# Kernel tuning notes

Measured on AMD Instinct MI355X. Metric: run time of the kernel, lower is better.

## Reference

```python
import jax, jax.numpy as jnp
import numpy as np
from jax import lax

WINDOW = 9
PAD = WINDOW // 2
LAMBDA_REG = 1.0
DN = lax.conv_dimension_numbers((1, 1, 1, 1, 1), (1, 1, 1, 1, 1), ('NCDHW', 'OIDHW', 'NCDHW'))


def _box_sum(x):
    """Sum over a 9x9x9 window with SAME padding, via separable 1D box filters.
    Mathematically identical to conv3d with an all-ones 9^3 kernel."""
    dtype = x.dtype
    for axis in range(3):  # D, H, W spatial axes
        kshape = [1, 1, 1, 1, 1]
        kshape[2 + axis] = WINDOW
        kernel = jnp.ones(kshape, dtype=dtype)
        padding = [(0, 0)] * 3
        padding[axis] = (PAD, PAD)
        x = lax.conv_general_dilated(x, kernel, window_strides=(1, 1, 1),
                                     padding=padding, dimension_numbers=DN)
    return x


def _lncc(I_fixed, I_moved):
    n = WINDOW ** 3
    fixed_sum = _box_sum(I_fixed)
    moved_sum = _box_sum(I_moved)
    fixed_mean = fixed_sum / n
    moved_mean = moved_sum / n
    fixed_sq = _box_sum(I_fixed * I_fixed)   # note: window SUM of squares (as in original)
    moved_sq = _box_sum(I_moved * I_moved)
    fixed_moved = _box_sum(I_fixed * I_moved)
    var_fixed = fixed_sq - fixed_mean ** 2
    var_moved = moved_sq - moved_mean ** 2
    cov = fixed_moved - fixed_mean * moved_mean
    cc = cov ** 2 / (var_fixed * var_moved + 1e-8)
    return -jnp.mean(cc)


def _gradient_loss(flow):
    dy = jnp.abs(flow[:, :, 1:, :, :] - flow[:, :, :-1, :, :])
    dx = jnp.abs(flow[:, :, :, 1:, :] - flow[:, :, :, :-1, :])
    dz = jnp.abs(flow[:, :, :, :, 1:] - flow[:, :, :, :, :-1])
    return jnp.mean(dx) + jnp.mean(dy) + jnp.mean(dz)


def setup_inputs() -> dict:
    key = jax.random.key(0)
    k1, k2, k3 = jax.random.split(key, 3)
    B, D, H, W = 2, 160, 192, 160
    I_fixed = jax.random.uniform(k1, (B, 1, D, H, W), dtype=jnp.float32)
    I_moved = jax.random.uniform(k2, (B, 1, D, H, W), dtype=jnp.float32)
    flow = jax.random.normal(k3, (B, 3, D, H, W), dtype=jnp.float32)
    return {"I_fixed": I_fixed, "I_moved": I_moved, "flow": flow}


def reference(I_fixed, I_moved, flow):
    L_sim = _lncc(I_fixed, I_moved)
    L_reg = _gradient_loss(flow)
    L_total = L_sim + LAMBDA_REG * L_reg
    return (L_total, L_sim, L_reg)
```

## Files before the change

kernel.cpp:

```cpp
#include <hip/hip_runtime.h>

#define Bz 2
#define Dz 160
#define Hz 192
#define Wz 160
#define HWl (Hz*Wz)
#define DHWl (Dz*Hz*Wz)

#define TH 16
#define TW 32
#define DT 32
#define RAWH (TH+8)
#define RAWW (TW+8)
#define NB_H (Hz/TH)
#define NB_W (Wz/TW)
#define NB_D (Dz/DT)
#define LNCC_BLOCKS (Bz*NB_H*NB_W*NB_D)
#define LNCC_THREADS 512
#define NSLICE (DT+8)

#define FLOW_BLOCKS 2048
#define FLOW_THREADS 256
#define FLOW_N4 ((Bz*3*DHWl)/4)

#define FPO LNCC_BLOCKS
#define WS_DOUBLES (FPO + 3*FLOW_BLOCKS)

__global__ __launch_bounds__(LNCC_THREADS, 2)
void lncc_kernel(const float* __restrict__ F, const float* __restrict__ M,
                 double* __restrict__ ws, int mode) {
    __shared__ float2 raw[RAWH][RAWW];
    __shared__ float4 wbv[RAWH][TW];
    __shared__ float  wbs[RAWH][TW];
    __shared__ double wred[LNCC_THREADS/64];

    const int bid = blockIdx.x;
    const int dc = bid % NB_D;
    const int wc = (bid / NB_D) % NB_W;
    const int hc = (bid / (NB_D * NB_W)) % NB_H;
    const int b  = bid / (NB_D * NB_W * NB_H);

    const int tid = threadIdx.x;
    const int th = tid >> 5;
    const int tw = tid & 31;

    const int h0 = hc * TH;
    const int w0 = wc * TW;
    const int d0 = dc * DT;
    const size_t bbase = (size_t)b * DHWl;

    float circ[9][5];
#pragma unroll
    for (int i = 0; i < 9; ++i)
#pragma unroll
        for (int j = 0; j < 5; ++j) circ[i][j] = 0.f;
    float rs0 = 0.f, rs1 = 0.f, rs2 = 0.f, rs3 = 0.f, rs4 = 0.f;
    float cc_acc = 0.f;

    for (int i0 = 0; i0 < NSLICE; i0 += 9) {
#pragma unroll
        for (int q = 0; q < 9; ++q) {
            const int i = i0 + q;
            if (i < NSLICE) {
                const int s = d0 - 4 + i;
                float nv0 = 0.f, nv1 = 0.f, nv2 = 0.f, nv3 = 0.f, nv4 = 0.f;
                if (s >= 0 && s < Dz) {
                    __syncthreads();
                    const size_t sbase = bbase + (size_t)s * HWl;
                    for (int k = tid; k < RAWH * RAWW; k += LNCC_THREADS) {
                        const int r = k / RAWW;
                        const int c = k - r * RAWW;
                        const int gh = h0 - 4 + r;
                        const int gw = w0 - 4 + c;
                        float fv = 0.f, mv = 0.f;
                        if (gh >= 0 && gh < Hz && gw >= 0 && gw < Wz) {
                            const size_t gi = sbase + (size_t)gh * Wz + gw;
                            fv = F[gi];
                            mv = M[gi];
                        }
                        raw[r][c] = make_float2(fv, mv);
                    }
                    __syncthreads();
                    for (int k = tid; k < RAWH * TW; k += LNCC_THREADS) {
                        const int r = k >> 5;
                        const int j = k & 31;
                        float sf = 0.f, sm = 0.f, sff = 0.f, smm = 0.f, sfm = 0.f;
#pragma unroll
                        for (int t = 0; t < 9; ++t) {
                            const float2 fm = raw[r][j + t];
                            sf  += fm.x;
                            sm  += fm.y;
                            sff += fm.x * fm.x;
                            smm += fm.y * fm.y;
                            sfm += fm.x * fm.y;
                        }
                        wbv[r][j] = make_float4(sf, sm, sff, smm);
                        wbs[r][j] = sfm;
                    }
                    __syncthreads();
#pragma unroll
                    for (int t = 0; t < 9; ++t) {
                        const float4 v = wbv[th + t][tw];
                        nv0 += v.x; nv1 += v.y; nv2 += v.z; nv3 += v.w;
                        nv4 += wbs[th + t][tw];
                    }
                }
                rs0 += nv0 - circ[q][0]; circ[q][0] = nv0;
                rs1 += nv1 - circ[q][1]; circ[q][1] = nv1;
                rs2 += nv2 - circ[q][2]; circ[q][2] = nv2;
                rs3 += nv3 - circ[q][3]; circ[q][3] = nv3;
                rs4 += nv4 - circ[q][4]; circ[q][4] = nv4;
                if (i >= 8) {
                    const float inv_n = 1.0f / 729.0f;
                    const float mf   = rs0 * inv_n;
                    const float mm   = rs1 * inv_n;
                    const float varf = rs2 - mf * mf;
                    const float varm = rs3 - mm * mm;
                    const float cov  = rs4 - mf * mm;
                    const float cc = cov * cov / (varf * varm + 1e-8f);
                    cc_acc += cc;
                }
            }
        }
    }

    double v = (double)cc_acc;
#pragma unroll
    for (int off = 32; off > 0; off >>= 1) v += __shfl_down(v, off);
    const int wave = tid >> 6, lane = tid & 63;
    if (lane == 0) wred[wave] = v;
    __syncthreads();
    if (tid == 0) {
        double t = 0.0;
        for (int k = 0; k < LNCC_THREADS / 64; ++k) t += wred[k];
        if (mode) ws[bid] = t;
        else      atomicAdd(&ws[0], t);
    }
}

__global__ __launch_bounds__(FLOW_THREADS)
void flow_grad_kernel(const float* __restrict__ X, double* __restrict__ ws, int mode) {
    __shared__ double wr0[4], wr1[4], wr2[4];
    float sd = 0.f, sh = 0.f, sw = 0.f;
    const int stride = gridDim.x * blockDim.x;
    for (int i4 = blockIdx.x * blockDim.x + threadIdx.x; i4 < FLOW_N4; i4 += stride) {
        const int base = i4 * 4;
        const float4 v = *(const float4*)(X + base);
        const int pos  = base % DHWl;
        const int w    = pos % Wz;
        const int rest = pos / Wz;
        const int h    = rest % Hz;
        const int d    = rest / Hz;
        float s = fabsf(v.y - v.x) + fabsf(v.z - v.y) + fabsf(v.w - v.z);
        if (w > 0) s += fabsf(v.x - X[base - 1]);
        sw += s;
        if (h > 0) {
            const float4 u = *(const float4*)(X + base - Wz);
            sh += fabsf(v.x - u.x) + fabsf(v.y - u.y) + fabsf(v.z - u.z) + fabsf(v.w - u.w);
        }
        if (d > 0) {
            const float4 u = *(const float4*)(X + base - HWl);
            sd += fabsf(v.x - u.x) + fabsf(v.y - u.y) + fabsf(v.z - u.z) + fabsf(v.w - u.w);
        }
    }
    double a = (double)sd, b = (double)sh, c = (double)sw;
#pragma unroll
    for (int off = 32; off > 0; off >>= 1) {
        a += __shfl_down(a, off);
        b += __shfl_down(b, off);
        c += __shfl_down(c, off);
    }
    const int wave = threadIdx.x >> 6, lane = threadIdx.x & 63;
    if (lane == 0) { wr0[wave] = a; wr1[wave] = b; wr2[wave] = c; }
    __syncthreads();
    if (threadIdx.x == 0) {
        double ta = 0.0, tb = 0.0, tc = 0.0;
        for (int k = 0; k < 4; ++k) { ta += wr0[k]; tb += wr1[k]; tc += wr2[k]; }
        if (mode) {
            double* p = ws + FPO + 3 * (size_t)blockIdx.x;
            p[0] = ta; p[1] = tb; p[2] = tc;
        } else {
            atomicAdd(&ws[1], ta);
            atomicAdd(&ws[2], tb);
            atomicAdd(&ws[3], tc);
        }
    }
}

__global__ __launch_bounds__(512)
void finalize_kernel(const double* __restrict__ ws, float* __restrict__ out, int mode) {
    __shared__ double red[4][8];
    double cc = 0.0, sd = 0.0, sh = 0.0, sw = 0.0;
    const int tid = threadIdx.x;
    if (mode) {
        for (int i = tid; i < LNCC_BLOCKS; i += 512) cc += ws[i];
        for (int i = tid; i < FLOW_BLOCKS; i += 512) {
            const double* p = ws + FPO + 3 * (size_t)i;
            sd += p[0]; sh += p[1]; sw += p[2];
        }
    } else if (tid == 0) {
        cc = ws[0]; sd = ws[1]; sh = ws[2]; sw = ws[3];
    }
#pragma unroll
    for (int off = 32; off > 0; off >>= 1) {
        cc += __shfl_down(cc, off);
        sd += __shfl_down(sd, off);
        sh += __shfl_down(sh, off);
        sw += __shfl_down(sw, off);
    }
    const int wave = tid >> 6, lane = tid & 63;
    if (lane == 0) { red[0][wave] = cc; red[1][wave] = sd; red[2][wave] = sh; red[3][wave] = sw; }
    __syncthreads();
    if (tid == 0) {
        double tcc = 0.0, tsd = 0.0, tsh = 0.0, tsw = 0.0;
        for (int k = 0; k < 8; ++k) {
            tcc += red[0][k]; tsd += red[1][k]; tsh += red[2][k]; tsw += red[3][k];
        }
        const double n_cc = 9830400.0;
        const double n_dx = 29337600.0;
        const double n_dy = 29306880.0;
        const double n_dz = 29306880.0;
        const double L_sim = -tcc / n_cc;
        const double L_reg = tsh / n_dx + tsd / n_dy + tsw / n_dz;
        out[0] = (float)(L_sim + L_reg);
        out[1] = (float)L_sim;
        out[2] = (float)L_reg;
    }
}

extern "C" void kernel_launch(void* const* d_in, const int* in_sizes, int n_in,
                              void* d_out, int out_size, void* d_ws, size_t ws_size,
                              hipStream_t stream) {
    (void)in_sizes; (void)n_in; (void)out_size;
    const float* F = (const float*)d_in[0];
    const float* M = (const float*)d_in[1];
    const float* X = (const float*)d_in[2];
    double* ws = (double*)d_ws;
    float* out = (float*)d_out;

    const int mode = (ws_size >= WS_DOUBLES * sizeof(double)) ? 1 : 0;
    if (!mode) hipMemsetAsync(d_ws, 0, 4 * sizeof(double), stream);

    lncc_kernel<<<LNCC_BLOCKS, LNCC_THREADS, 0, stream>>>(F, M, ws, mode);
    flow_grad_kernel<<<FLOW_BLOCKS, FLOW_THREADS, 0, stream>>>(X, ws, mode);
    finalize_kernel<<<1, 512, 0, stream>>>(ws, out, mode);
}
```

Measured before the change: 375.2 us.

## Shrink LNCC tiles for more blocks and use bucketed atomic reductions

The LNCC kernel now uses 16x16 tiles in H/W, a depth chunk of 20 and 256-thread blocks, with a higher occupancy hint. That gives many more blocks and better load balance across CUs, at the cost of more halo overhead per tile: the W halo grows from 8/32 to 8/16 and the D halo from 8/32 to 8/20. The per-block workspace partials are replaced by atomic adds into up to 64 striped buckets, and the finalize kernel shrinks to a single wave. The workspace is now always cleared with a memset before launch.

```diff
diff --git a/kernel.cpp b/kernel.cpp
--- a/kernel.cpp
+++ b/kernel.cpp
@@ -8,27 +8,26 @@
 #define DHWl (Dz*Hz*Wz)
 
 #define TH 16
-#define TW 32
-#define DT 32
+#define TW 16
+#define DT 20
 #define RAWH (TH+8)
 #define RAWW (TW+8)
 #define NB_H (Hz/TH)
 #define NB_W (Wz/TW)
 #define NB_D (Dz/DT)
 #define LNCC_BLOCKS (Bz*NB_H*NB_W*NB_D)
-#define LNCC_THREADS 512
+#define LNCC_THREADS 256
 #define NSLICE (DT+8)
 
 #define FLOW_BLOCKS 2048
 #define FLOW_THREADS 256
 #define FLOW_N4 ((Bz*3*DHWl)/4)
 
-#define FPO LNCC_BLOCKS
-#define WS_DOUBLES (FPO + 3*FLOW_BLOCKS)
-
-__global__ __launch_bounds__(LNCC_THREADS, 2)
+#define MAXBUCK 64
+
+__global__ __launch_bounds__(LNCC_THREADS, 6)
 void lncc_kernel(const float* __restrict__ F, const float* __restrict__ M,
-                 double* __restrict__ ws, int mode) {
+                 double* __restrict__ ws, int nbuck) {
     __shared__ float2 raw[RAWH][RAWW];
     __shared__ float4 wbv[RAWH][TW];
     __shared__ float  wbs[RAWH][TW];
@@ -41,8 +40,8 @@
     const int b  = bid / (NB_D * NB_W * NB_H);
 
     const int tid = threadIdx.x;
-    const int th = tid >> 5;
-    const int tw = tid & 31;
+    const int th = tid >> 4;
+    const int tw = tid & 15;
 
     const int h0 = hc * TH;
     const int w0 = wc * TW;
@@ -82,8 +81,8 @@
                     }
                     __syncthreads();
                     for (int k = tid; k < RAWH * TW; k += LNCC_THREADS) {
-                        const int r = k >> 5;
-                        const int j = k & 31;
+                        const int r = k >> 4;
+                        const int j = k & 15;
                         float sf = 0.f, sm = 0.f, sff = 0.f, smm = 0.f, sfm = 0.f;
 #pragma unroll
                         for (int t = 0; t < 9; ++t) {
@@ -133,13 +132,13 @@
     if (tid == 0) {
         double t = 0.0;
         for (int k = 0; k < LNCC_THREADS / 64; ++k) t += wred[k];
-        if (mode) ws[bid] = t;
-        else      atomicAdd(&ws[0], t);
+        const int bucket = bid % nbuck;
+        atomicAdd(&ws[bucket * 4 + 0], t);
     }
 }
 
 __global__ __launch_bounds__(FLOW_THREADS)
-void flow_grad_kernel(const float* __restrict__ X, double* __restrict__ ws, int mode) {
+void flow_grad_kernel(const float* __restrict__ X, double* __restrict__ ws, int nbuck) {
     __shared__ double wr0[4], wr1[4], wr2[4];
     float sd = 0.f, sh = 0.f, sw = 0.f;
     const int stride = gridDim.x * blockDim.x;
@@ -176,30 +175,21 @@
     if (threadIdx.x == 0) {
         double ta = 0.0, tb = 0.0, tc = 0.0;
         for (int k = 0; k < 4; ++k) { ta += wr0[k]; tb += wr1[k]; tc += wr2[k]; }
-        if (mode) {
-            double* p = ws + FPO + 3 * (size_t)blockIdx.x;
-            p[0] = ta; p[1] = tb; p[2] = tc;
-        } else {
-            atomicAdd(&ws[1], ta);
-            atomicAdd(&ws[2], tb);
-            atomicAdd(&ws[3], tc);
-        }
-    }
-}
-
-__global__ __launch_bounds__(512)
-void finalize_kernel(const double* __restrict__ ws, float* __restrict__ out, int mode) {
-    __shared__ double red[4][8];
+        const int bucket = (int)(blockIdx.x % (unsigned)nbuck);
+        double* p = ws + bucket * 4;
+        atomicAdd(&p[1], ta);
+        atomicAdd(&p[2], tb);
+        atomicAdd(&p[3], tc);
+    }
+}
+
+__global__ __launch_bounds__(64)
+void finalize_kernel(const double* __restrict__ ws, float* __restrict__ out, int nbuck) {
+    const int tid = threadIdx.x;
     double cc = 0.0, sd = 0.0, sh = 0.0, sw = 0.0;
-    const int tid = threadIdx.x;
-    if (mode) {
-        for (int i = tid; i < LNCC_BLOCKS; i += 512) cc += ws[i];
-        for (int i = tid; i < FLOW_BLOCKS; i += 512) {
-            const double* p = ws + FPO + 3 * (size_t)i;
-            sd += p[0]; sh += p[1]; sw += p[2];
-        }
-    } else if (tid == 0) {
-        cc = ws[0]; sd = ws[1]; sh = ws[2]; sw = ws[3];
+    if (tid < nbuck) {
+        const double* p = ws + tid * 4;
+        cc = p[0]; sd = p[1]; sh = p[2]; sw = p[3];
     }
 #pragma unroll
     for (int off = 32; off > 0; off >>= 1) {
@@ -208,20 +198,13 @@
         sh += __shfl_down(sh, off);
         sw += __shfl_down(sw, off);
     }
-    const int wave = tid >> 6, lane = tid & 63;
-    if (lane == 0) { red[0][wave] = cc; red[1][wave] = sd; red[2][wave] = sh; red[3][wave] = sw; }
-    __syncthreads();
     if (tid == 0) {
-        double tcc = 0.0, tsd = 0.0, tsh = 0.0, tsw = 0.0;
-        for (int k = 0; k < 8; ++k) {
-            tcc += red[0][k]; tsd += red[1][k]; tsh += red[2][k]; tsw += red[3][k];
-        }
         const double n_cc = 9830400.0;
         const double n_dx = 29337600.0;
         const double n_dy = 29306880.0;
         const double n_dz = 29306880.0;
-        const double L_sim = -tcc / n_cc;
-        const double L_reg = tsh / n_dx + tsd / n_dy + tsw / n_dz;
+        const double L_sim = -cc / n_cc;
+        const double L_reg = sh / n_dx + sd / n_dy + sw / n_dz;
         out[0] = (float)(L_sim + L_reg);
         out[1] = (float)L_sim;
         out[2] = (float)L_reg;
@@ -238,10 +221,12 @@
     double* ws = (double*)d_ws;
     float* out = (float*)d_out;
 
-    const int mode = (ws_size >= WS_DOUBLES * sizeof(double)) ? 1 : 0;
-    if (!mode) hipMemsetAsync(d_ws, 0, 4 * sizeof(double), stream);
-
-    lncc_kernel<<<LNCC_BLOCKS, LNCC_THREADS, 0, stream>>>(F, M, ws, mode);
-    flow_grad_kernel<<<FLOW_BLOCKS, FLOW_THREADS, 0, stream>>>(X, ws, mode);
-    finalize_kernel<<<1, 512, 0, stream>>>(ws, out, mode);
-}
+    int nbuck = (int)(ws_size / (4 * sizeof(double)));
+    if (nbuck > MAXBUCK) nbuck = MAXBUCK;
+    if (nbuck < 1) nbuck = 1;
+
+    hipMemsetAsync(d_ws, 0, (size_t)nbuck * 4 * sizeof(double), stream);
+    lncc_kernel<<<LNCC_BLOCKS, LNCC_THREADS, 0, stream>>>(F, M, ws, nbuck);
+    flow_grad_kernel<<<FLOW_BLOCKS, FLOW_THREADS, 0, stream>>>(X, ws, nbuck);
+    finalize_kernel<<<1, 64, 0, stream>>>(ws, out, nbuck);
+}
```

Result: slower. 445.3 us (+18.7%).
